# Kernel optimization log

Hardware: AMD Instinct MI355X
Metric: run time of the kernel (lower is better)

The kernel has to match this reference:

```python
import jax, jax.numpy as jnp
import numpy as np

B, S, H = 4, 2048, 1024
E, K, F = 8, 2, 4096


def setup_inputs() -> dict:
    key = jax.random.key(0)
    ks = jax.random.split(key, 6)
    x = jax.random.normal(ks[0], (B, S, H), dtype=jnp.float32)
    gate_w = jax.random.normal(ks[1], (H, E), dtype=jnp.float32) * 0.02
    w1 = jax.random.normal(ks[2], (E, H, F), dtype=jnp.float32) * 0.02
    b1 = jnp.zeros((E, F), dtype=jnp.float32)
    w2 = jax.random.normal(ks[3], (E, F, H), dtype=jnp.float32) * 0.02
    b2 = jnp.zeros((E, H), dtype=jnp.float32)
    return {"x": x, "gate_w": gate_w, "w1": w1, "b1": b1, "w2": w2, "b2": b2}


def reference(x, gate_w, w1, b1, w2, b2):
    # NOTE: the torch module masks expert inputs per token, but since each
    # expert's output is re-masked by the same mask, the math is exactly
    # out[t] = sum_i renorm_prob[t,i] * expert_{topk_idx[t,i]}(x[t]).
    # Dropout is identity in eval mode.
    T = B * S
    x_flat = x.reshape(T, H)

    gate_scores = x_flat @ gate_w                      # [T, E]
    gate_probs = jax.nn.softmax(gate_scores, axis=-1)  # [T, E]
    topk_vals, topk_idx = jax.lax.top_k(gate_probs, K)  # [T, K]
    topk_w = jax.nn.softmax(topk_vals, axis=-1)        # renormalize via softmax (as in source)

    # Combine weights per (token, expert): sum over top-k slots.
    onehot = jax.nn.one_hot(topk_idx, E, dtype=x.dtype)           # [T, K, E]
    comb = jnp.einsum('tk,tke->te', topk_w, onehot)               # [T, E]

    # Run all experts densely (faithful to naive module; combine masks out unrouted).
    h = jnp.einsum('th,ehf->etf', x_flat, w1) + b1[:, None, :]    # [E, T, F]
    h = jax.nn.relu(h)
    expert_out = jnp.einsum('etf,efh->eth', h, w2) + b2[:, None, :]  # [E, T, H]

    out_flat = jnp.einsum('te,eth->th', comb, expert_out)         # [T, H]
    output = out_flat.reshape(B, S, H)

    # Load-balance loss: KL(uniform || softmax(mean gate prob)), batchmean over E.
    expert_usage = gate_probs.mean(axis=0)                        # [E]
    log_sm = jax.nn.log_softmax(expert_usage, axis=0)
    uniform = jnp.full((E,), 1.0 / E, dtype=x.dtype)
    kl = jnp.sum(uniform * (jnp.log(uniform) - log_sm)) / E
    load_balance_loss = 0.01 * kl
    return output, load_balance_loss
```

## Files before the change

### kernel.cpp

```cpp
#include <hip/hip_runtime.h>
#include <stdint.h>

#define T_TOK 8192
#define HD 1024
#define NE 8
#define FD 4096
#define RALLOC 18432
#define G1 1152
#define G2 384
#define NKT1 16
#define GATE_BLOCKS 1024
#define TP1_BLOCKS 4096

typedef __attribute__((ext_vector_type(8))) short bf16x8;
typedef __attribute__((ext_vector_type(4))) float f32x4;
typedef __attribute__((ext_vector_type(4))) short s16x4;

__device__ __forceinline__ unsigned short f2bf(float f) {
  unsigned u = __builtin_bit_cast(unsigned, f);
  u += 0x7fffu + ((u >> 16) & 1u);
  return (unsigned short)(u >> 16);
}

__device__ __forceinline__ void gld_lds16(const void* g, void* l) {
  __builtin_amdgcn_global_load_lds(
      (const __attribute__((address_space(1))) void*)g,
      (__attribute__((address_space(3))) void*)l, 16, 0, 0);
}

__global__ __launch_bounds__(512) void k_prep1(const float* __restrict__ w1,
                                               unsigned short* __restrict__ w1t,
                                               const float* __restrict__ x,
                                               const float* __restrict__ gw,
                                               int* __restrict__ toke,
                                               float* __restrict__ tokw,
                                               int* __restrict__ counts8,
                                               double* __restrict__ part,
                                               unsigned short* __restrict__ xbf) {
  __shared__ char smem[33312];
  const int id = blockIdx.x;
  const int tid = threadIdx.x;
  if (id < TP1_BLOCKS) {
    const int half = tid >> 8;
    const int t2 = tid & 255;
    unsigned short* tile = (unsigned short*)(smem + half * 10240);
    const int tt = id * 2 + half;
    const int e = tt >> 10, rem = tt & 1023;
    const int R = HD, C = FD;
    const int r0 = (rem >> 6) << 6, c0 = (rem & 63) << 6;
    const float* src = w1 + (size_t)e * R * C;
    unsigned short* dst = w1t + (size_t)e * R * C;
    {
      const int r = t2 >> 2, cg = (t2 & 3) * 16;
      #pragma unroll
      for (int m = 0; m < 4; ++m) {
        float4 v = *(const float4*)(src + (size_t)(r0 + r) * C + c0 + cg + 4 * m);
        s16x4 pv;
        pv[0] = (short)f2bf(v.x); pv[1] = (short)f2bf(v.y);
        pv[2] = (short)f2bf(v.z); pv[3] = (short)f2bf(v.w);
        *(s16x4*)&tile[r * 80 + cg + 4 * m] = pv;
      }
    }
    __syncthreads();
    {
      const int c = t2 >> 2, rg = (t2 & 3) * 16;
      bf16x8 v0, v1;
      #pragma unroll
      for (int j = 0; j < 8; ++j) v0[j] = (short)tile[(rg + j) * 80 + c];
      #pragma unroll
      for (int j = 0; j < 8; ++j) v1[j] = (short)tile[(rg + 8 + j) * 80 + c];
      unsigned short* dp = dst + (size_t)(c0 + c) * R + r0 + rg;
      *(bf16x8*)dp = v0;
      *(bf16x8*)(dp + 8) = v1;
    }
    return;
  }
  float* gwT = (float*)smem;
  double (*sp)[8] = (double(*)[8])(smem + 32768);
  int* scnt = (int*)(smem + 33280);
  const int gb = id - TP1_BLOCKS;
  const int lane = tid & 63;
  const int w = tid >> 6;
  if (tid < 8) scnt[tid] = 0;
  #pragma unroll
  for (int rep = 0; rep < 16; ++rep) {
    int idx = rep * 512 + tid;
    gwT[(idx & 7) * 1024 + (idx >> 3)] = gw[idx];
  }
  __syncthreads();

  const int t = gb * 8 + w;
  double acc[8];
  #pragma unroll
  for (int e = 0; e < 8; ++e) acc[e] = 0.0;
  const float* xr = x + (size_t)t * HD;
  unsigned short* xbr = xbf + (size_t)t * HD;
  #pragma unroll
  for (int j = 0; j < 4; ++j) {
    const int hh = j * 256 + lane * 4;
    float4 xv = *(const float4*)(xr + hh);
    s16x4 pv;
    pv[0] = (short)f2bf(xv.x); pv[1] = (short)f2bf(xv.y);
    pv[2] = (short)f2bf(xv.z); pv[3] = (short)f2bf(xv.w);
    *(s16x4*)(xbr + hh) = pv;
    #pragma unroll
    for (int e = 0; e < 8; ++e) {
      float4 gv = *(const float4*)(gwT + e * 1024 + hh);
      acc[e] += (double)xv.x * (double)gv.x;
      acc[e] += (double)xv.y * (double)gv.y;
      acc[e] += (double)xv.z * (double)gv.z;
      acc[e] += (double)xv.w * (double)gv.w;
    }
  }
  for (int off = 32; off > 0; off >>= 1) {
    #pragma unroll
    for (int e = 0; e < 8; ++e) acc[e] += __shfl_xor(acc[e], off, 64);
  }
  double m = acc[0];
  #pragma unroll
  for (int e = 1; e < 8; ++e) m = fmax(m, acc[e]);
  double p[8], ssum = 0.0;
  #pragma unroll
  for (int e = 0; e < 8; ++e) { p[e] = exp(acc[e] - m); ssum += p[e]; }
  double inv = 1.0 / ssum;
  #pragma unroll
  for (int e = 0; e < 8; ++e) p[e] *= inv;
  int e0 = 0;
  #pragma unroll
  for (int e = 1; e < 8; ++e) if (p[e] > p[e0]) e0 = e;
  int e1 = (e0 == 0) ? 1 : 0;
  #pragma unroll
  for (int e = 0; e < 8; ++e) if (e != e0 && p[e] > p[e1]) e1 = e;
  if (lane == 0) {
    double z = exp(p[e1] - p[e0]);
    double w0 = 1.0 / (1.0 + z);
    toke[2 * t] = e0; toke[2 * t + 1] = e1;
    tokw[2 * t] = (float)w0; tokw[2 * t + 1] = (float)(z / (1.0 + z));
    atomicAdd(&scnt[e0], 1);
    atomicAdd(&scnt[e1], 1);
    #pragma unroll
    for (int e = 0; e < 8; ++e) sp[w][e] = p[e];
  }
  __syncthreads();
  if (tid < 8) {
    double s = 0.0;
    #pragma unroll
    for (int q = 0; q < 8; ++q) s += sp[q][tid];
    part[(size_t)gb * 8 + tid] = s;
    counts8[(size_t)gb * 8 + tid] = scnt[tid];
  }
}

__global__ __launch_bounds__(256) void k_scan(const int* __restrict__ counts8,
                                              int* __restrict__ offs,
                                              int* __restrict__ cursors,
                                              const double* __restrict__ part,
                                              float* __restrict__ loss_out,
                                              int* __restrict__ rowmap,
                                              float* __restrict__ roww) {
  __shared__ double su[8];
  __shared__ int soffs[9];
  __shared__ int scnt[8];
  const int tid = threadIdx.x;
  const int e = tid >> 5, sub = tid & 31;
  double s = 0.0;
  int c = 0;
  for (int b = sub; b < GATE_BLOCKS; b += 32) {
    s += part[(size_t)b * 8 + e];
    c += counts8[(size_t)b * 8 + e];
  }
  for (int off = 16; off > 0; off >>= 1) {
    s += __shfl_xor(s, off, 64);
    c += __shfl_xor(c, off, 64);
  }
  if (sub == 0) { su[e] = s; scnt[e] = c; }
  __syncthreads();
  if (tid == 0) {
    int o = 0;
    for (int i = 0; i < 8; ++i) {
      soffs[i] = o; offs[i] = o; cursors[i * 16] = o;
      o += ((scnt[i] + 255) >> 8) << 8;
    }
    soffs[8] = o; offs[8] = o;
    double u[8], mx = -1e300;
    for (int i = 0; i < 8; ++i) { u[i] = su[i] / 8192.0; mx = fmax(mx, u[i]); }
    double se = 0.0;
    for (int i = 0; i < 8; ++i) se += exp(u[i] - mx);
    double lse = mx + log(se);
    double kl = 0.0;
    const double lu = log(0.125);
    for (int i = 0; i < 8; ++i) kl += 0.125 * (lu - (u[i] - lse));
    kl /= 8.0;
    loss_out[0] = (float)(0.01 * kl);
  }
  __syncthreads();
  for (int i = 0; i < 8; ++i) {
    int s0 = soffs[i] + scnt[i];
    int en = soffs[i + 1];
    for (int k = s0 + tid; k < en; k += 256) { rowmap[k] = 2 * T_TOK; roww[k] = 0.f; }
  }
}

__global__ __launch_bounds__(256) void k_scatter(const int* __restrict__ toke,
                                                 const float* __restrict__ tokw,
                                                 int* __restrict__ cursors,
                                                 int* __restrict__ rowmap,
                                                 float* __restrict__ roww) {
  const int t = blockIdx.x * 256 + threadIdx.x;
  const int lane = threadIdx.x & 63;
  #pragma unroll
  for (int k = 0; k < 2; ++k) {
    int e = toke[2 * t + k];
    float wv = tokw[2 * t + k];
    for (int ex = 0; ex < 8; ++ex) {
      unsigned long long mask = __ballot(e == ex);
      if (e == ex) {
        int leader = __ffsll((unsigned long long)mask) - 1;
        int rank = __popcll(mask & ((1ull << lane) - 1ull));
        int base = 0;
        if (lane == leader) base = atomicAdd(&cursors[ex * 16], __popcll(mask));
        base = __shfl(base, leader, 64);
        rowmap[base + rank] = 2 * t + k;
        roww[base + rank] = wv;
      }
    }
  }
}

#define RDA(buf, mh) do { _Pragma("unroll") for (int m_ = 0; m_ < 4; ++m_) { \
  af[m_][0] = *(const bf16x8*)(lds + (buf) * 65536 + wmOff + (mh) * 8192 + aoff[m_][0]); \
  af[m_][1] = *(const bf16x8*)(lds + (buf) * 65536 + wmOff + (mh) * 8192 + aoff[m_][1]); } } while (0)

#define RDB(buf, nh, B) do { _Pragma("unroll") for (int nf_ = 0; nf_ < 2; ++nf_) { \
  B[nf_][0] = *(const bf16x8*)(lds + (buf) * 65536 + wnOff + (nh) * 4096 + boff[nf_][0]); \
  B[nf_][1] = *(const bf16x8*)(lds + (buf) * 65536 + wnOff + (nh) * 4096 + boff[nf_][1]); } } while (0)

#define MMA(mh, nh, B) do { _Pragma("unroll") for (int m_ = 0; m_ < 4; ++m_) \
  _Pragma("unroll") for (int nf_ = 0; nf_ < 2; ++nf_) \
  _Pragma("unroll") for (int kh_ = 0; kh_ < 2; ++kh_) \
    acc[(mh) * 4 + m_][(nh) * 2 + nf_] = __builtin_amdgcn_mfma_f32_16x16x32_bf16( \
        af[m_][kh_], B[nf_][kh_], acc[(mh) * 4 + m_][(nh) * 2 + nf_], 0, 0, 0); } while (0)

#define SYNC_PRE() do { __builtin_amdgcn_sched_barrier(0); __builtin_amdgcn_s_barrier(); \
  asm volatile("s_waitcnt lgkmcnt(0)" ::: "memory"); __builtin_amdgcn_sched_barrier(0); \
  __builtin_amdgcn_s_setprio(1); } while (0)

#define SYNC_POST() do { __builtin_amdgcn_s_setprio(0); __builtin_amdgcn_sched_barrier(0); \
  __builtin_amdgcn_s_barrier(); __builtin_amdgcn_sched_barrier(0); } while (0)

#define SYNC_POST_VM() do { __builtin_amdgcn_s_setprio(0); __builtin_amdgcn_sched_barrier(0); \
  asm volatile("s_waitcnt vmcnt(4)" ::: "memory"); __builtin_amdgcn_sched_barrier(0); \
  __builtin_amdgcn_s_barrier(); __builtin_amdgcn_sched_barrier(0); } while (0)

#define FRAG_OFFSETS256() \
  int aoff[4][2], boff[2][2]; \
  { \
    const int kg = (lane >> 4) << 4; \
    _Pragma("unroll") \
    for (int m = 0; m < 4; ++m) { \
      int r = m * 16 + (lane & 15); \
      _Pragma("unroll") \
      for (int kh = 0; kh < 2; ++kh) \
        aoff[m][kh] = r * 128 + ((kh * 64 + kg) ^ ((r & 7) << 4)); \
    } \
    _Pragma("unroll") \
    for (int nf = 0; nf < 2; ++nf) { \
      int r = (wn & 1) * 64 + nf * 16 + (lane & 15); \
      _Pragma("unroll") \
      for (int kh = 0; kh < 2; ++kh) \
        boff[nf][kh] = r * 128 + ((kh * 64 + kg) ^ ((r & 7) << 4)); \
    } \
  }

__global__ __launch_bounds__(512, 2) void k_gemm1(const unsigned short* __restrict__ xbf,
                                                  const unsigned short* __restrict__ w1t,
                                                  const float* __restrict__ b1,
                                                  const int* __restrict__ rowmap,
                                                  const int* __restrict__ offs,
                                                  unsigned short* __restrict__ hbuf,
                                                  const float* __restrict__ w2,
                                                  unsigned short* __restrict__ w2t) {
  __shared__ char lds[131072];
  const int id = blockIdx.x;
  const int tid = threadIdx.x;
  if (id >= G1) {
    const int half = tid >> 8;
    const int t2 = tid & 255;
    unsigned short* tile = (unsigned short*)(lds + half * 10240);
    const int tt = (id - G1) * 2 + half;
    const int e = tt >> 10, rem = tt & 1023;
    const int R = FD, C = HD;
    const int r0 = (rem >> 4) << 6, c0 = (rem & 15) << 6;
    const float* src = w2 + (size_t)e * R * C;
    unsigned short* dst = w2t + (size_t)e * R * C;
    {
      const int r = t2 >> 2, cg = (t2 & 3) * 16;
      #pragma unroll
      for (int m = 0; m < 4; ++m) {
        float4 v = *(const float4*)(src + (size_t)(r0 + r) * C + c0 + cg + 4 * m);
        s16x4 pv;
        pv[0] = (short)f2bf(v.x); pv[1] = (short)f2bf(v.y);
        pv[2] = (short)f2bf(v.z); pv[3] = (short)f2bf(v.w);
        *(s16x4*)&tile[r * 80 + cg + 4 * m] = pv;
      }
    }
    __syncthreads();
    {
      const int c = t2 >> 2, rg = (t2 & 3) * 16;
      bf16x8 v0, v1;
      #pragma unroll
      for (int j = 0; j < 8; ++j) v0[j] = (short)tile[(rg + j) * 80 + c];
      #pragma unroll
      for (int j = 0; j < 8; ++j) v1[j] = (short)tile[(rg + 8 + j) * 80 + c];
      unsigned short* dp = dst + (size_t)(c0 + c) * R + r0 + rg;
      *(bf16x8*)dp = v0;
      *(bf16x8*)(dp + 8) = v1;
    }
    return;
  }
  const int xcd = id & 7, l = id >> 3;
  const int ntr = offs[8] >> 8;
  const int nj = ntr * 16;
  const int q = nj >> 3, r8 = nj & 7;
  const int cnt = q + (xcd < r8 ? 1 : 0);
  if (l >= cnt) return;
  const int start = (xcd < r8) ? xcd * (q + 1) : r8 * (q + 1) + (xcd - r8) * q;
  const int g = start + l;
  const int rt = g >> 4, nb = g & 15;
  const int row0 = rt * 256;
  int e = 0;
  #pragma unroll
  for (int i = 1; i < 8; ++i) if (row0 >= offs[i]) e = i;
  const int n0 = nb * 256;
  const int lane = tid & 63;
  const int wid = tid >> 6;
  const int wm = wid >> 2, wn = wid & 3;

  const int rl = tid >> 3;
  const int cbs = ((tid & 7) << 4) ^ ((rl & 7) << 4);
  const char* pA[2][2];
  #pragma unroll
  for (int h = 0; h < 2; ++h)
    #pragma unroll
    for (int l2 = 0; l2 < 2; ++l2) {
      int tok = rowmap[row0 + h * 128 + l2 * 64 + rl] >> 1;
      pA[h][l2] = (const char*)xbf + (size_t)tok * 2048 + cbs;
    }
  const char* pB00 = (const char*)w1t + (size_t)e * ((size_t)FD * HD * 2) +
                     (size_t)(n0 + rl) * 2048 + cbs;
  const int stw = wid * 1024;

#define STA1(buf, h, kt) do { \
  gld_lds16(pA[h][0] + (size_t)(kt) * 128, lds + (buf) * 65536 + (h) * 16384 + stw); \
  gld_lds16(pA[h][1] + (size_t)(kt) * 128, lds + (buf) * 65536 + (h) * 16384 + 8192 + stw); } while (0)
#define STB1(buf, h, kt) do { \
  gld_lds16(pB00 + (size_t)(h) * 128 * 2048 + (size_t)(kt) * 128, \
            lds + (buf) * 65536 + 32768 + (h) * 16384 + stw); \
  gld_lds16(pB00 + ((size_t)(h) * 128 + 64) * 2048 + (size_t)(kt) * 128, \
            lds + (buf) * 65536 + 32768 + (h) * 16384 + 8192 + stw); } while (0)

  FRAG_OFFSETS256();
  const int wmOff = wm * 16384;
  const int wnOff = 32768 + (wn >> 1) * 16384;

  f32x4 acc[8][4];
  #pragma unroll
  for (int a = 0; a < 8; ++a)
    #pragma unroll
    for (int b = 0; b < 4; ++b) acc[a][b] = (f32x4){0.f, 0.f, 0.f, 0.f};
  bf16x8 af[4][2], b0r[2][2], b1r[2][2];

  STA1(0, 0, 0); STA1(0, 1, 0); STB1(0, 0, 0); STB1(0, 1, 0);
  STB1(1, 0, 1); STB1(1, 1, 1);
  asm volatile("s_waitcnt vmcnt(4)" ::: "memory");
  __builtin_amdgcn_sched_barrier(0);
  __builtin_amdgcn_s_barrier();
  __builtin_amdgcn_sched_barrier(0);

  #pragma unroll 1
  for (int i = 0; i < NKT1 / 2; ++i) {
    const int k1 = 2 * i + 1, k2 = 2 * i + 2, k3 = 2 * i + 3;
    RDA(0, 0); RDB(0, 0, b0r); STA1(1, 0, k1); SYNC_PRE(); MMA(0, 0, b0r); SYNC_POST();
    RDB(0, 1, b1r);            STA1(1, 1, k1); SYNC_PRE(); MMA(0, 1, b1r); SYNC_POST();
    RDA(0, 1);                 STB1(0, 0, k2); SYNC_PRE(); MMA(1, 1, b1r); SYNC_POST();
                               STB1(0, 1, k2); SYNC_PRE(); MMA(1, 0, b0r); SYNC_POST_VM();
    RDA(1, 0); RDB(1, 0, b0r); STA1(0, 0, k2); SYNC_PRE(); MMA(0, 0, b0r); SYNC_POST();
    RDB(1, 1, b1r);            STA1(0, 1, k2); SYNC_PRE(); MMA(0, 1, b1r); SYNC_POST();
    RDA(1, 1);                 STB1(1, 0, k3); SYNC_PRE(); MMA(1, 1, b1r); SYNC_POST();
                               STB1(1, 1, k3); SYNC_PRE(); MMA(1, 0, b0r); SYNC_POST_VM();
  }

  asm volatile("s_waitcnt vmcnt(0)" ::: "memory");
  __builtin_amdgcn_sched_barrier(0);
  __syncthreads();
  #pragma unroll
  for (int na = 0; na < 4; ++na) {
    int c = wn * 64 + (na >> 1) * 32 + (na & 1) * 16 + (lane & 15);
    float bias = b1[(size_t)e * FD + n0 + c];
    #pragma unroll
    for (int ma = 0; ma < 8; ++ma) {
      #pragma unroll
      for (int j2 = 0; j2 < 4; ++j2) {
        int r = wm * 128 + (ma >> 2) * 64 + (ma & 3) * 16 + ((lane >> 4) << 2) + j2;
        float v = fmaxf(acc[ma][na][j2] + bias, 0.f);
        *(unsigned short*)(lds + r * 512 + ((c * 2) ^ ((r & 7) << 4))) = f2bf(v);
      }
    }
  }
  __syncthreads();
  #pragma unroll
  for (int s = 0; s < 16; ++s) {
    int flat = s * 512 + tid;
    int r = flat >> 5, ch = flat & 31;
    bf16x8 v = *(const bf16x8*)(lds + r * 512 + ((ch * 16) ^ ((r & 7) << 4)));
    *(bf16x8*)((char*)hbuf + (size_t)(row0 + r) * 8192 + (size_t)n0 * 2 + ch * 16) = v;
  }
#undef STA1
#undef STB1
}

__global__ __launch_bounds__(512, 2) void k_gemm2(const unsigned short* __restrict__ hbuf,
                                                  const unsigned short* __restrict__ w2t,
                                                  const float* __restrict__ b2,
                                                  const int* __restrict__ rowmap,
                                                  const float* __restrict__ roww,
                                                  const int* __restrict__ offs,
                                                  float* __restrict__ out2,
                                                  float* __restrict__ psplit) {
  __shared__ char lds[131072];
  const int id = blockIdx.x;
  int bx, by, kt0, niter, jj = -1;
  if (id < 256) {
    const int sid = (id & 7) * 32 + (id >> 3);
    bx = sid & 3; by = sid >> 2;
    kt0 = 0; niter = 32;
  } else {
    const int jid = id - 256;
    const int q = (jid & 7) * 16 + (jid >> 3);
    const int t = 256 + (q >> 2);
    const int nT2 = (offs[8] >> 8) * 4;
    if (t >= nT2) return;
    bx = t & 3; by = t >> 2;
    kt0 = (q & 3) * 16; niter = 8;
    jj = q;
  }
  const int row0 = by * 256;
  int e = 0;
  #pragma unroll
  for (int i = 1; i < 8; ++i) if (row0 >= offs[i]) e = i;
  const int n0 = bx * 256;
  const int tid = threadIdx.x;
  const int lane = tid & 63;
  const int wid = tid >> 6;
  const int wm = wid >> 2, wn = wid & 3;

  const int rl = tid >> 3;
  const int cbs = ((tid & 7) << 4) ^ ((rl & 7) << 4);
  const char* pA00 = (const char*)hbuf + (size_t)(row0 + rl) * 8192 + cbs;
  const char* pB00 = (const char*)w2t + (size_t)e * ((size_t)HD * FD * 2) +
                     (size_t)(n0 + rl) * 8192 + cbs;
  const int stw = wid * 1024;

#define STA2(buf, h, kt) do { \
  gld_lds16(pA00 + (size_t)(h) * 128 * 8192 + (size_t)(kt) * 128, \
            lds + (buf) * 65536 + (h) * 16384 + stw); \
  gld_lds16(pA00 + ((size_t)(h) * 128 + 64) * 8192 + (size_t)(kt) * 128, \
            lds + (buf) * 65536 + (h) * 16384 + 8192 + stw); } while (0)
#define STB2(buf, h, kt) do { \
  gld_lds16(pB00 + (size_t)(h) * 128 * 8192 + (size_t)(kt) * 128, \
            lds + (buf) * 65536 + 32768 + (h) * 16384 + stw); \
  gld_lds16(pB00 + ((size_t)(h) * 128 + 64) * 8192 + (size_t)(kt) * 128, \
            lds + (buf) * 65536 + 32768 + (h) * 16384 + 8192 + stw); } while (0)

  FRAG_OFFSETS256();
  const int wmOff = wm * 16384;
  const int wnOff = 32768 + (wn >> 1) * 16384;

  f32x4 acc[8][4];
  #pragma unroll
  for (int a = 0; a < 8; ++a)
    #pragma unroll
    for (int b = 0; b < 4; ++b) acc[a][b] = (f32x4){0.f, 0.f, 0.f, 0.f};
  bf16x8 af[4][2], b0r[2][2], b1r[2][2];

  STA2(0, 0, kt0); STA2(0, 1, kt0); STB2(0, 0, kt0); STB2(0, 1, kt0);
  STB2(1, 0, kt0 + 1); STB2(1, 1, kt0 + 1);
  asm volatile("s_waitcnt vmcnt(4)" ::: "memory");
  __builtin_amdgcn_sched_barrier(0);
  __builtin_amdgcn_s_barrier();
  __builtin_amdgcn_sched_barrier(0);

  #pragma unroll 1
  for (int i = 0; i < niter; ++i) {
    const int k1 = kt0 + 2 * i + 1, k2 = kt0 + 2 * i + 2, k3 = kt0 + 2 * i + 3;
    RDA(0, 0); RDB(0, 0, b0r); STA2(1, 0, k1); SYNC_PRE(); MMA(0, 0, b0r); SYNC_POST();
    RDB(0, 1, b1r);            STA2(1, 1, k1); SYNC_PRE(); MMA(0, 1, b1r); SYNC_POST();
    RDA(0, 1);                 STB2(0, 0, k2); SYNC_PRE(); MMA(1, 1, b1r); SYNC_POST();
                               STB2(0, 1, k2); SYNC_PRE(); MMA(1, 0, b0r); SYNC_POST_VM();
    RDA(1, 0); RDB(1, 0, b0r); STA2(0, 0, k2); SYNC_PRE(); MMA(0, 0, b0r); SYNC_POST();
    RDB(1, 1, b1r);            STA2(0, 1, k2); SYNC_PRE(); MMA(0, 1, b1r); SYNC_POST();
    RDA(1, 1);                 STB2(1, 0, k3); SYNC_PRE(); MMA(1, 1, b1r); SYNC_POST();
                               STB2(1, 1, k3); SYNC_PRE(); MMA(1, 0, b0r); SYNC_POST_VM();
  }

  asm volatile("s_waitcnt vmcnt(0)" ::: "memory");
  __builtin_amdgcn_sched_barrier(0);
  if (jj < 0) {
    #pragma unroll
    for (int ma = 0; ma < 8; ++ma) {
      #pragma unroll
      for (int j2 = 0; j2 < 4; ++j2) {
        int r = wm * 128 + (ma >> 2) * 64 + (ma & 3) * 16 + ((lane >> 4) << 2) + j2;
        int rm = rowmap[row0 + r];
        float wr = roww[row0 + r];
        float* orow = out2 + (size_t)rm * 1024 + n0;
        #pragma unroll
        for (int na = 0; na < 4; ++na) {
          int c = wn * 64 + (na >> 1) * 32 + (na & 1) * 16 + (lane & 15);
          orow[c] = (acc[ma][na][j2] + b2[(size_t)e * HD + n0 + c]) * wr;
        }
      }
    }
  } else {
    float* ps = psplit + (size_t)jj * 65536;
    #pragma unroll
    for (int ma = 0; ma < 8; ++ma) {
      #pragma unroll
      for (int j2 = 0; j2 < 4; ++j2) {
        int r = wm * 128 + (ma >> 2) * 64 + (ma & 3) * 16 + ((lane >> 4) << 2) + j2;
        #pragma unroll
        for (int na = 0; na < 4; ++na) {
          int c = wn * 64 + (na >> 1) * 32 + (na & 1) * 16 + (lane & 15);
          ps[r * 256 + c] = acc[ma][na][j2];
        }
      }
    }
  }
#undef STA2
#undef STB2
}

__global__ __launch_bounds__(512) void k_fix2(const float* __restrict__ psplit,
                                              const int* __restrict__ offs,
                                              const float* __restrict__ b2,
                                              const int* __restrict__ rowmap,
                                              const float* __restrict__ roww,
                                              float* __restrict__ out2) {
  const int nT2 = (offs[8] >> 8) * 4;
  const int t = 256 + blockIdx.x;
  if (t >= nT2) return;
  const int by = t >> 2, bx = t & 3;
  const int row0 = by * 256, n0 = bx * 256;
  int e = 0;
  #pragma unroll
  for (int i = 1; i < 8; ++i) if (row0 >= offs[i]) e = i;
  const float* ps = psplit + (size_t)blockIdx.x * 4 * 65536;
  const int cg = (threadIdx.x & 63) * 4;
  const int r0t = threadIdx.x >> 6;
  float4 bb = *(const float4*)(b2 + (size_t)e * HD + n0 + cg);
  for (int rr = 0; rr < 32; ++rr) {
    int r = rr * 8 + r0t;
    int rm = rowmap[row0 + r];
    float wr = roww[row0 + r];
    float4 s0 = *(const float4*)(ps + 0 * 65536 + r * 256 + cg);
    float4 s1 = *(const float4*)(ps + 1 * 65536 + r * 256 + cg);
    float4 s2 = *(const float4*)(ps + 2 * 65536 + r * 256 + cg);
    float4 s3 = *(const float4*)(ps + 3 * 65536 + r * 256 + cg);
    float4 o;
    o.x = wr * (s0.x + s1.x + s2.x + s3.x + bb.x);
    o.y = wr * (s0.y + s1.y + s2.y + s3.y + bb.y);
    o.z = wr * (s0.z + s1.z + s2.z + s3.z + bb.z);
    o.w = wr * (s0.w + s1.w + s2.w + s3.w + bb.w);
    *(float4*)(out2 + (size_t)rm * 1024 + n0 + cg) = o;
  }
}

__global__ __launch_bounds__(256) void k_combine(const float* __restrict__ out2,
                                                 float* __restrict__ out) {
  const int t = blockIdx.x;
  const int i = threadIdx.x * 4;
  float4 a = *(const float4*)(out2 + (size_t)(2 * t) * 1024 + i);
  float4 b = *(const float4*)(out2 + (size_t)(2 * t + 1) * 1024 + i);
  float4 r;
  r.x = a.x + b.x; r.y = a.y + b.y; r.z = a.z + b.z; r.w = a.w + b.w;
  *(float4*)(out + (size_t)t * 1024 + i) = r;
}

extern "C" void kernel_launch(void* const* d_in, const int* in_sizes, int n_in,
                              void* d_out, int out_size, void* d_ws, size_t ws_size,
                              hipStream_t stream) {
  const float* x = (const float*)d_in[0];
  const float* gw = (const float*)d_in[1];
  const float* w1 = (const float*)d_in[2];
  const float* b1 = (const float*)d_in[3];
  const float* w2 = (const float*)d_in[4];
  const float* b2 = (const float*)d_in[5];
  float* out = (float*)d_out;

  char* ws = (char*)d_ws;
  size_t o = 0;
  unsigned short* w2t = (unsigned short*)(ws + o); o += (size_t)NE * HD * FD * 2;
  unsigned short* hbuf = (unsigned short*)(ws + o); o += (size_t)RALLOC * FD * 2;
  unsigned short* w1t = (unsigned short*)(ws + o);
  size_t w1t_off = o; o += (size_t)NE * FD * HD * 2;
  unsigned short* xbf = (unsigned short*)(ws + o); o += (size_t)T_TOK * HD * 2;
  int* rowmap = (int*)(ws + o); o += (size_t)RALLOC * 4;
  float* roww = (float*)(ws + o); o += (size_t)RALLOC * 4;
  int* toke = (int*)(ws + o); o += (size_t)T_TOK * 2 * 4;
  float* tokw = (float*)(ws + o); o += (size_t)T_TOK * 2 * 4;
  double* part = (double*)(ws + o); o += (size_t)GATE_BLOCKS * 8 * 8;
  int* counts8 = (int*)(ws + o); o += (size_t)GATE_BLOCKS * 8 * 4;
  int* ctrl = (int*)(ws + o); o += 1024;
  int* offs = ctrl;
  int* cursors = ctrl + 64;
  float* psplit = (float*)(ws + o); o += (size_t)128 * 65536 * 4;
  float* out2 = (float*)(ws + w1t_off);

  k_prep1<<<TP1_BLOCKS + GATE_BLOCKS, 512, 0, stream>>>(w1, w1t, x, gw, toke, tokw,
                                                        counts8, part, xbf);
  k_scan<<<1, 256, 0, stream>>>(counts8, offs, cursors, part, out + (size_t)T_TOK * HD,
                                rowmap, roww);
  k_scatter<<<T_TOK / 256, 256, 0, stream>>>(toke, tokw, cursors, rowmap, roww);
  k_gemm1<<<G1 + 4096, 512, 0, stream>>>(xbf, w1t, b1, rowmap, offs, hbuf, w2, w2t);
  k_gemm2<<<G2, 512, 0, stream>>>(hbuf, w2t, b2, rowmap, roww, offs, out2, psplit);
  k_fix2<<<32, 512, 0, stream>>>(psplit, offs, b2, rowmap, roww, out2);
  k_combine<<<T_TOK, 256, 0, stream>>>(out2, out);
}
```

Baseline: 453.0 us.

## Fuse scan into scatter kernel and deepen split-K for gemm2 tail tiles

Merges the single-block scan and the scatter kernel into one launch. Every block recomputes the per-expert counts and offsets redundantly, and the cursors now start at zero after a memset. Separately, the gemm2 tail tiles switch from a 4-way to an 8-way K split, with a larger partial buffer and an 8-way reduction in the fix-up kernel. The aim is to cut a launch and the serial scan latency, and to keep more CUs busy during the gemm2 tail, at the cost of redundant count reads and more partial-sum traffic.

```diff
diff --git a/kernel.cpp b/kernel.cpp
--- a/kernel.cpp
+++ b/kernel.cpp
@@ -7,7 +7,7 @@
 #define FD 4096
 #define RALLOC 18432
 #define G1 1152
-#define G2 384
+#define G2 512
 #define NKT1 16
 #define GATE_BLOCKS 1024
 #define TP1_BLOCKS 4096
@@ -151,77 +151,79 @@
   }
 }
 
-__global__ __launch_bounds__(256) void k_scan(const int* __restrict__ counts8,
-                                              int* __restrict__ offs,
-                                              int* __restrict__ cursors,
-                                              const double* __restrict__ part,
-                                              float* __restrict__ loss_out,
-                                              int* __restrict__ rowmap,
-                                              float* __restrict__ roww) {
-  __shared__ double su[8];
+__global__ __launch_bounds__(256) void k_scansc(const int* __restrict__ counts8,
+                                                int* __restrict__ offs,
+                                                int* __restrict__ cursors,
+                                                const double* __restrict__ part,
+                                                float* __restrict__ loss_out,
+                                                int* __restrict__ rowmap,
+                                                float* __restrict__ roww,
+                                                const int* __restrict__ toke,
+                                                const float* __restrict__ tokw) {
   __shared__ int soffs[9];
   __shared__ int scnt[8];
+  __shared__ double su[8];
   const int tid = threadIdx.x;
   const int e = tid >> 5, sub = tid & 31;
-  double s = 0.0;
   int c = 0;
-  for (int b = sub; b < GATE_BLOCKS; b += 32) {
-    s += part[(size_t)b * 8 + e];
-    c += counts8[(size_t)b * 8 + e];
-  }
-  for (int off = 16; off > 0; off >>= 1) {
-    s += __shfl_xor(s, off, 64);
-    c += __shfl_xor(c, off, 64);
-  }
-  if (sub == 0) { su[e] = s; scnt[e] = c; }
+  for (int b = sub; b < GATE_BLOCKS; b += 32) c += counts8[(size_t)b * 8 + e];
+  for (int off = 16; off > 0; off >>= 1) c += __shfl_xor(c, off, 64);
+  if (sub == 0) scnt[e] = c;
   __syncthreads();
   if (tid == 0) {
     int o = 0;
     for (int i = 0; i < 8; ++i) {
-      soffs[i] = o; offs[i] = o; cursors[i * 16] = o;
+      soffs[i] = o;
       o += ((scnt[i] + 255) >> 8) << 8;
     }
-    soffs[8] = o; offs[8] = o;
-    double u[8], mx = -1e300;
-    for (int i = 0; i < 8; ++i) { u[i] = su[i] / 8192.0; mx = fmax(mx, u[i]); }
-    double se = 0.0;
-    for (int i = 0; i < 8; ++i) se += exp(u[i] - mx);
-    double lse = mx + log(se);
-    double kl = 0.0;
-    const double lu = log(0.125);
-    for (int i = 0; i < 8; ++i) kl += 0.125 * (lu - (u[i] - lse));
-    kl /= 8.0;
-    loss_out[0] = (float)(0.01 * kl);
+    soffs[8] = o;
   }
   __syncthreads();
-  for (int i = 0; i < 8; ++i) {
-    int s0 = soffs[i] + scnt[i];
-    int en = soffs[i + 1];
-    for (int k = s0 + tid; k < en; k += 256) { rowmap[k] = 2 * T_TOK; roww[k] = 0.f; }
-  }
-}
-
-__global__ __launch_bounds__(256) void k_scatter(const int* __restrict__ toke,
-                                                 const float* __restrict__ tokw,
-                                                 int* __restrict__ cursors,
-                                                 int* __restrict__ rowmap,
-                                                 float* __restrict__ roww) {
-  const int t = blockIdx.x * 256 + threadIdx.x;
-  const int lane = threadIdx.x & 63;
+
+  if (blockIdx.x == 0) {
+    double s = 0.0;
+    for (int b = sub; b < GATE_BLOCKS; b += 32) s += part[(size_t)b * 8 + e];
+    for (int off = 16; off > 0; off >>= 1) s += __shfl_xor(s, off, 64);
+    if (sub == 0) su[e] = s;
+    __syncthreads();
+    if (tid == 0) {
+      for (int i = 0; i < 9; ++i) offs[i] = soffs[i];
+      double u[8], mx = -1e300;
+      for (int i = 0; i < 8; ++i) { u[i] = su[i] / 8192.0; mx = fmax(mx, u[i]); }
+      double se = 0.0;
+      for (int i = 0; i < 8; ++i) se += exp(u[i] - mx);
+      double lse = mx + log(se);
+      double kl = 0.0;
+      const double lu = log(0.125);
+      for (int i = 0; i < 8; ++i) kl += 0.125 * (lu - (u[i] - lse));
+      kl /= 8.0;
+      loss_out[0] = (float)(0.01 * kl);
+    }
+    __syncthreads();
+    for (int i = 0; i < 8; ++i) {
+      int s0 = soffs[i] + scnt[i];
+      int en = soffs[i + 1];
+      for (int k = s0 + tid; k < en; k += 256) { rowmap[k] = 2 * T_TOK; roww[k] = 0.f; }
+    }
+    return;
+  }
+  const int t = (blockIdx.x - 1) * 256 + tid;
+  const int lane = tid & 63;
   #pragma unroll
   for (int k = 0; k < 2; ++k) {
-    int e = toke[2 * t + k];
+    int te = toke[2 * t + k];
     float wv = tokw[2 * t + k];
     for (int ex = 0; ex < 8; ++ex) {
-      unsigned long long mask = __ballot(e == ex);
-      if (e == ex) {
+      unsigned long long mask = __ballot(te == ex);
+      if (te == ex) {
         int leader = __ffsll((unsigned long long)mask) - 1;
         int rank = __popcll(mask & ((1ull << lane) - 1ull));
         int base = 0;
         if (lane == leader) base = atomicAdd(&cursors[ex * 16], __popcll(mask));
         base = __shfl(base, leader, 64);
-        rowmap[base + rank] = 2 * t + k;
-        roww[base + rank] = wv;
+        int slot = soffs[ex] + base + rank;
+        rowmap[slot] = 2 * t + k;
+        roww[slot] = wv;
       }
     }
   }
@@ -436,12 +438,12 @@
     kt0 = 0; niter = 32;
   } else {
     const int jid = id - 256;
-    const int q = (jid & 7) * 16 + (jid >> 3);
-    const int t = 256 + (q >> 2);
+    const int q = (jid & 7) * 32 + (jid >> 3);
+    const int t = 256 + (q >> 3);
     const int nT2 = (offs[8] >> 8) * 4;
     if (t >= nT2) return;
     bx = t & 3; by = t >> 2;
-    kt0 = (q & 3) * 16; niter = 8;
+    kt0 = (q & 7) * 8; niter = 4;
     jj = q;
   }
   const int row0 = by * 256;
@@ -554,7 +556,7 @@
   int e = 0;
   #pragma unroll
   for (int i = 1; i < 8; ++i) if (row0 >= offs[i]) e = i;
-  const float* ps = psplit + (size_t)blockIdx.x * 4 * 65536;
+  const float* ps = psplit + (size_t)blockIdx.x * 8 * 65536;
   const int cg = (threadIdx.x & 63) * 4;
   const int r0t = threadIdx.x >> 6;
   float4 bb = *(const float4*)(b2 + (size_t)e * HD + n0 + cg);
@@ -562,15 +564,14 @@
     int r = rr * 8 + r0t;
     int rm = rowmap[row0 + r];
     float wr = roww[row0 + r];
-    float4 s0 = *(const float4*)(ps + 0 * 65536 + r * 256 + cg);
-    float4 s1 = *(const float4*)(ps + 1 * 65536 + r * 256 + cg);
-    float4 s2 = *(const float4*)(ps + 2 * 65536 + r * 256 + cg);
-    float4 s3 = *(const float4*)(ps + 3 * 65536 + r * 256 + cg);
+    float4 s = bb;
+    #pragma unroll
+    for (int k = 0; k < 8; ++k) {
+      float4 v = *(const float4*)(ps + (size_t)k * 65536 + r * 256 + cg);
+      s.x += v.x; s.y += v.y; s.z += v.z; s.w += v.w;
+    }
     float4 o;
-    o.x = wr * (s0.x + s1.x + s2.x + s3.x + bb.x);
-    o.y = wr * (s0.y + s1.y + s2.y + s3.y + bb.y);
-    o.z = wr * (s0.z + s1.z + s2.z + s3.z + bb.z);
-    o.w = wr * (s0.w + s1.w + s2.w + s3.w + bb.w);
+    o.x = wr * s.x; o.y = wr * s.y; o.z = wr * s.z; o.w = wr * s.w;
     *(float4*)(out2 + (size_t)rm * 1024 + n0 + cg) = o;
   }
 }
@@ -613,14 +614,14 @@
   int* ctrl = (int*)(ws + o); o += 1024;
   int* offs = ctrl;
   int* cursors = ctrl + 64;
-  float* psplit = (float*)(ws + o); o += (size_t)128 * 65536 * 4;
+  float* psplit = (float*)(ws + o); o += (size_t)256 * 65536 * 4;
   float* out2 = (float*)(ws + w1t_off);
 
+  hipMemsetAsync(ctrl, 0, 1024, stream);
   k_prep1<<<TP1_BLOCKS + GATE_BLOCKS, 512, 0, stream>>>(w1, w1t, x, gw, toke, tokw,
                                                         counts8, part, xbf);
-  k_scan<<<1, 256, 0, stream>>>(counts8, offs, cursors, part, out + (size_t)T_TOK * HD,
-                                rowmap, roww);
-  k_scatter<<<T_TOK / 256, 256, 0, stream>>>(toke, tokw, cursors, rowmap, roww);
+  k_scansc<<<33, 256, 0, stream>>>(counts8, offs, cursors, part,
+                                   out + (size_t)T_TOK * HD, rowmap, roww, toke, tokw);
   k_gemm1<<<G1 + 4096, 512, 0, stream>>>(xbf, w1t, b1, rowmap, offs, hbuf, w2, w2t);
   k_gemm2<<<G2, 512, 0, stream>>>(hbuf, w2t, b2, rowmap, roww, offs, out2, psplit);
   k_fix2<<<32, 512, 0, stream>>>(psplit, offs, b2, rowmap, roww, out2);
```

Result: no change. 456.5 us (+0.8%).
